# Kernel tuning notes

Hardware: AMD Instinct MI355X
Metric: run time of the kernel (lower is better)

The kernel has to match this reference:

```python
import jax, jax.numpy as jnp
import numpy as np

C = 384
NUM_HEADS = 12
WS = 12  # window side
N = WS * WS  # tokens per window = 144
NW = 144  # windows per image
BATCH = 8

def setup_inputs() -> dict:
    key = jax.random.key(0)
    k1, k2, k3, k4, k5, k6, k7 = jax.random.split(key, 7)
    x = jax.random.normal(k1, (BATCH, NW, WS, WS, C), dtype=jnp.float32)
    mask = jax.random.normal(k2, (NW, N, N), dtype=jnp.float32)
    s = 1.0 / np.sqrt(C)
    qkv_w = jax.random.normal(k3, (3 * C, C), dtype=jnp.float32) * s
    qkv_b = jax.random.normal(k4, (3 * C,), dtype=jnp.float32) * 0.02
    proj_w = jax.random.normal(k5, (C, C), dtype=jnp.float32) * s
    proj_b = jax.random.normal(k6, (C,), dtype=jnp.float32) * 0.02
    return {"x": x, "mask": mask, "qkv_w": qkv_w, "qkv_b": qkv_b,
            "proj_w": proj_w, "proj_b": proj_b}

def reference(x, mask, qkv_w, qkv_b, proj_w, proj_b):
    B, nW = x.shape[0], x.shape[1]
    head_dim = C // NUM_HEADS
    scale = head_dim ** -0.5
    # (B_, N, C) windowed tokens
    xw = x.reshape(B * nW, N, C)
    qkv = jnp.einsum('bnc,dc->bnd', xw, qkv_w) + qkv_b  # (B_, N, 3C)
    qkv = qkv.reshape(B * nW, N, 3, NUM_HEADS, head_dim)
    q = qkv[:, :, 0].transpose(0, 2, 1, 3) * scale  # (B_, H, N, hd)
    k = qkv[:, :, 1].transpose(0, 2, 1, 3)
    v = qkv[:, :, 2].transpose(0, 2, 1, 3)
    attn = jnp.einsum('bhnd,bhmd->bhnm', q, k)  # (B_, H, N, N)
    # add window mask: view as (B, nW, H, N, N) + mask[None, :, None]
    attn = attn.reshape(B, nW, NUM_HEADS, N, N) + mask[None, :, None, :, :]
    attn = jax.nn.softmax(attn.reshape(B * nW, NUM_HEADS, N, N), axis=-1)
    out = jnp.einsum('bhnm,bhmd->bhnd', attn, v)  # (B_, H, N, hd)
    out = out.transpose(0, 2, 1, 3).reshape(B * nW, N, C)
    out = jnp.einsum('bnc,dc->bnd', out, proj_w) + proj_b
    return out
```

## Files before the change

kernel.cpp:

```cpp
#include <hip/hip_runtime.h>
#include <stdint.h>

#define TOK 144
#define CD  384
#define NH  12
#define HDIM 32
#define NWIN 1152
#define MASKW 144
#define NQKV 1152

typedef __bf16 bf16_t;
typedef __bf16 bf16x4 __attribute__((ext_vector_type(4)));
typedef __bf16 bf16x8 __attribute__((ext_vector_type(8)));
typedef float  f32x4  __attribute__((ext_vector_type(4)));

__device__ __forceinline__ void gload16(const void* g, void* l) {
    __builtin_amdgcn_global_load_lds(
        (const __attribute__((address_space(1))) uint32_t*)g,
        (__attribute__((address_space(3))) uint32_t*)l, 16, 0, 0);
}

__global__ __launch_bounds__(256) void kconv(const float* __restrict__ qkvw,
                                             const float* __restrict__ projw,
                                             bf16_t* __restrict__ wq,
                                             bf16_t* __restrict__ wp)
{
    int i = (blockIdx.x * 256 + threadIdx.x) * 4;
    const int NQ = NQKV * CD;
    if (i < NQ) {
        float4 v = *(const float4*)(qkvw + i);
        bf16x4 o = {(bf16_t)v.x, (bf16_t)v.y, (bf16_t)v.z, (bf16_t)v.w};
        *(bf16x4*)(wq + i) = o;
    } else {
        int j = i - NQ;
        if (j < CD * CD) {
            float4 v = *(const float4*)(projw + j);
            bf16x4 o = {(bf16_t)v.x, (bf16_t)v.y, (bf16_t)v.z, (bf16_t)v.w};
            *(bf16x4*)(wp + j) = o;
        }
    }
}

__global__ __launch_bounds__(256) void kx(const float* __restrict__ x,
                                          bf16_t* __restrict__ xb, int n8)
{
    int i = blockIdx.x * 256 + threadIdx.x;
    if (i < n8) {
        float4 a = *(const float4*)(x + (size_t)i * 8);
        float4 b = *(const float4*)(x + (size_t)i * 8 + 4);
        bf16x8 o = {(bf16_t)a.x, (bf16_t)a.y, (bf16_t)a.z, (bf16_t)a.w,
                    (bf16_t)b.x, (bf16_t)b.y, (bf16_t)b.z, (bf16_t)b.w};
        *(bf16x8*)(xb + (size_t)i * 8) = o;
    }
}

__global__ __launch_bounds__(256) void k_qkv(const bf16_t* __restrict__ xb,
                                             const bf16_t* __restrict__ wB,
                                             const float* __restrict__ bias,
                                             bf16_t* __restrict__ Qp,
                                             bf16_t* __restrict__ Kp,
                                             bf16_t* __restrict__ VTp)
{
    int nwg = gridDim.x;
    int orig = blockIdx.x;
    int q8 = nwg >> 3, r8 = nwg & 7;
    int xcd = orig & 7, idx = orig >> 3;
    int wgid = (xcd < r8 ? xcd * (q8 + 1) : r8 * (q8 + 1) + (xcd - r8) * q8) + idx;
    int mb = wgid / 9, nb = wgid % 9;

    __shared__ union SMem {
        struct { bf16_t A[128 * 64]; bf16_t B[128 * 64]; } st;
        bf16_t tile[128 * 136];
    } sm;
    bf16_t* As = sm.st.A;
    bf16_t* Bs = sm.st.B;

    int tid = threadIdx.x;
    int lane = tid & 63, wid = tid >> 6;
    int wr = (wid >> 1) * 64, wc = (wid & 1) * 64;
    int l15 = lane & 15, l4 = lane >> 4;
    int lr8 = lane >> 3, lc8 = lane & 7;

    f32x4 acc[4][4] = {};

    const size_t arow0 = (size_t)mb * 128;
    const bf16_t* aG = xb + (arow0 + (size_t)(wid * 4) * 8 + lr8) * 384 + lc8 * 8;
    const bf16_t* bG = wB + ((size_t)nb * 128 + (size_t)(wid * 4) * 8 + lr8) * 384 + lc8 * 8;

    for (int kk = 0; kk < 6; ++kk) {
        #pragma unroll
        for (int p = 0; p < 4; ++p)
            gload16(aG + (size_t)p * (8 * 384) + kk * 64, As + (wid * 4 + p) * 512);
        #pragma unroll
        for (int p = 0; p < 4; ++p)
            gload16(bG + (size_t)p * (8 * 384) + kk * 64, Bs + (wid * 4 + p) * 512);
        __syncthreads();

        #pragma unroll
        for (int kh = 0; kh < 2; ++kh) {
            bf16x8 af[4], bfr[4];
            #pragma unroll
            for (int i = 0; i < 4; ++i)
                af[i] = *(const bf16x8*)&As[(wr + i * 16 + l15) * 64 + kh * 32 + l4 * 8];
            #pragma unroll
            for (int j = 0; j < 4; ++j)
                bfr[j] = *(const bf16x8*)&Bs[(wc + j * 16 + l15) * 64 + kh * 32 + l4 * 8];
            #pragma unroll
            for (int i = 0; i < 4; ++i)
                #pragma unroll
                for (int j = 0; j < 4; ++j)
                    acc[i][j] = __builtin_amdgcn_mfma_f32_16x16x32_bf16(af[i], bfr[j], acc[i][j], 0, 0, 0);
        }
        __syncthreads();
    }

    const int S = 136;
    const float SCALE = 0.17677669529663687f;
    float scl = (nb < 3) ? SCALE : 1.0f;
    float bv[4];
    #pragma unroll
    for (int j = 0; j < 4; ++j) bv[j] = bias[nb * 128 + wc + j * 16 + l15];

    #pragma unroll
    for (int i = 0; i < 4; ++i)
        #pragma unroll
        for (int j = 0; j < 4; ++j)
            #pragma unroll
            for (int r = 0; r < 4; ++r)
                sm.tile[(wr + i * 16 + l4 * 4 + r) * S + wc + j * 16 + l15] =
                    (bf16_t)((acc[i][j][r] + bv[j]) * scl);
    __syncthreads();

    if (nb < 6) {
        bf16_t* dst = (nb < 3) ? Qp : Kp;
        int db0 = (nb % 3) * 128;
        #pragma unroll
        for (int it = 0; it < 8; ++it) {
            int item = tid + it * 256;
            int row = item >> 4, ch = item & 15;
            bf16x8 v = *(const bf16x8*)&sm.tile[row * S + ch * 8];
            int gr = mb * 128 + row;
            int lw = gr / 144, n = gr - lw * 144;
            int dl = db0 + ch * 8;
            int h = dl >> 5, c32 = dl & 31;
            *(bf16x8*)(dst + (size_t)(lw * 12 + h) * 4608 + n * 32 + c32) = v;
        }
    } else {
        int db0 = (nb - 6) * 128;
        #pragma unroll
        for (int it = 0; it < 8; ++it) {
            int item = tid + it * 256;
            int dl = item & 127;
            int nc = item >> 7;
            int gr0 = mb * 128 + nc * 8;
            int lw = gr0 / 144, n0 = gr0 - lw * 144;
            int rr = db0 + dl;
            int h = rr >> 5, j32 = rr & 31;
            bf16x8 v;
            #pragma unroll
            for (int q = 0; q < 8; ++q)
                v[q] = sm.tile[(nc * 8 + q) * S + dl];
            *(bf16x8*)(VTp + (size_t)(lw * 12 + h) * 4608 + j32 * 144 + n0) = v;
        }
    }
}

__global__ __launch_bounds__(576) void k_attn(const bf16_t* __restrict__ Qp,
                                              const bf16_t* __restrict__ Kp,
                                              const bf16_t* __restrict__ VTp,
                                              const float* __restrict__ mask,
                                              bf16_t* __restrict__ ao,
                                              int w0)
{
    extern __shared__ char smem[];
    bf16_t* kb  = (bf16_t*)smem;
    bf16_t* vtb = kb + 144 * 40;
    bf16_t* pb  = vtb + 32 * 168;

    int bw = blockIdx.x / 12, h = blockIdx.x % 12;
    int W = w0 + bw;
    size_t base = (size_t)(bw * 12 + h) * 4608;
    int tid = threadIdx.x;

    {
        int row = tid >> 2, c8 = (tid & 3) * 8;
        *(uint4*)&kb[row * 40 + c8] = *(const uint4*)(Kp + base + row * 32 + c8);
        int j = tid / 18, seg = tid % 18;
        *(uint4*)&vtb[j * 168 + seg * 8] = *(const uint4*)(VTp + base + j * 144 + seg * 8);
        if (tid < 64) {
            int jj = tid >> 1, cc = 144 + (tid & 1) * 8;
            uint4 z = {0, 0, 0, 0};
            *(uint4*)&vtb[jj * 168 + cc] = z;
        }
    }
    __syncthreads();

    int lane = tid & 63, wv = tid >> 6;
    int l15 = lane & 15, l4 = lane >> 4;
    int row16 = wv * 16;
    const f32x4 fzero = {0.f, 0.f, 0.f, 0.f};

    bf16x8 aq = *(const bf16x8*)(Qp + base + (row16 + l15) * 32 + l4 * 8);
    f32x4 s[9];
    #pragma unroll
    for (int nt = 0; nt < 9; ++nt) {
        bf16x8 bk = *(const bf16x8*)&kb[(nt * 16 + l15) * 40 + l4 * 8];
        s[nt] = __builtin_amdgcn_mfma_f32_16x16x32_bf16(aq, bk, fzero, 0, 0, 0);
    }
    const float* mrow = mask + (size_t)(W % MASKW) * (144 * 144);
    #pragma unroll
    for (int nt = 0; nt < 9; ++nt)
        #pragma unroll
        for (int r = 0; r < 4; ++r)
            s[nt][r] += mrow[(row16 + l4 * 4 + r) * 144 + nt * 16 + l15];

    float mx[4], sm[4];
    #pragma unroll
    for (int r = 0; r < 4; ++r) {
        float m = s[0][r];
        #pragma unroll
        for (int nt = 1; nt < 9; ++nt) m = fmaxf(m, s[nt][r]);
        #pragma unroll
        for (int off = 1; off < 16; off <<= 1) m = fmaxf(m, __shfl_xor(m, off, 64));
        mx[r] = m;
    }
    #pragma unroll
    for (int r = 0; r < 4; ++r) {
        float sum = 0.f;
        #pragma unroll
        for (int nt = 0; nt < 9; ++nt) {
            float e = __expf(s[nt][r] - mx[r]);
            s[nt][r] = e;
            sum += e;
        }
        #pragma unroll
        for (int off = 1; off < 16; off <<= 1) sum += __shfl_xor(sum, off, 64);
        sm[r] = sum;
    }

    #pragma unroll
    for (int nt = 0; nt < 9; ++nt)
        #pragma unroll
        for (int r = 0; r < 4; ++r)
            pb[(row16 + l4 * 4 + r) * 168 + nt * 16 + l15] = (bf16_t)s[nt][r];
    {
        int rr = lane >> 2, cc = 144 + (lane & 3) * 4;
        uint2 z = {0, 0};
        *(uint2*)&pb[(row16 + rr) * 168 + cc] = z;
    }
    f32x4 o0 = {0.f, 0.f, 0.f, 0.f}, o1 = {0.f, 0.f, 0.f, 0.f};
    #pragma unroll
    for (int ks = 0; ks < 5; ++ks) {
        bf16x8 ap  = *(const bf16x8*)&pb[(row16 + l15) * 168 + ks * 32 + l4 * 8];
        bf16x8 bv0 = *(const bf16x8*)&vtb[(l15) * 168 + ks * 32 + l4 * 8];
        bf16x8 bv1 = *(const bf16x8*)&vtb[(16 + l15) * 168 + ks * 32 + l4 * 8];
        o0 = __builtin_amdgcn_mfma_f32_16x16x32_bf16(ap, bv0, o0, 0, 0, 0);
        o1 = __builtin_amdgcn_mfma_f32_16x16x32_bf16(ap, bv1, o1, 0, 0, 0);
    }
    float inv[4];
    #pragma unroll
    for (int r = 0; r < 4; ++r) inv[r] = 1.0f / sm[r];
    bf16_t* ob = pb + row16 * 168;
    #pragma unroll
    for (int r = 0; r < 4; ++r) {
        ob[(l4 * 4 + r) * 32 + l15]      = (bf16_t)(o0[r] * inv[r]);
        ob[(l4 * 4 + r) * 32 + 16 + l15] = (bf16_t)(o1[r] * inv[r]);
    }
    bf16x8 v = *(const bf16x8*)&ob[(lane >> 2) * 32 + (lane & 3) * 8];
    *(bf16x8*)(ao + ((size_t)bw * 144 + row16 + (lane >> 2)) * 384 + h * 32 + (lane & 3) * 8) = v;
}

__global__ __launch_bounds__(256) void k_proj(const bf16_t* __restrict__ ao,
                                              const bf16_t* __restrict__ wp,
                                              const float* __restrict__ bias,
                                              float* __restrict__ out,
                                              int rowoff)
{
    int nwg = gridDim.x;
    int orig = blockIdx.x;
    int q8 = nwg >> 3, r8 = nwg & 7;
    int xcd = orig & 7, idx = orig >> 3;
    int wgid = (xcd < r8 ? xcd * (q8 + 1) : r8 * (q8 + 1) + (xcd - r8) * q8) + idx;
    int mb = wgid / 3, nb = wgid % 3;

    __shared__ union SMem {
        struct { bf16_t A[128 * 64]; bf16_t B[128 * 64]; } st;
        float tile[128 * 68];
    } sm;
    bf16_t* As = sm.st.A;
    bf16_t* Bs = sm.st.B;

    int tid = threadIdx.x;
    int lane = tid & 63, wid = tid >> 6;
    int wr = (wid >> 1) * 64, wc = (wid & 1) * 64;
    int l15 = lane & 15, l4 = lane >> 4;
    int lr8 = lane >> 3, lc8 = lane & 7;

    f32x4 acc[4][4] = {};

    const bf16_t* aG = ao + ((size_t)mb * 128 + (size_t)(wid * 4) * 8 + lr8) * 384 + lc8 * 8;
    const bf16_t* bG = wp + ((size_t)nb * 128 + (size_t)(wid * 4) * 8 + lr8) * 384 + lc8 * 8;

    for (int kk = 0; kk < 6; ++kk) {
        #pragma unroll
        for (int p = 0; p < 4; ++p)
            gload16(aG + (size_t)p * (8 * 384) + kk * 64, As + (wid * 4 + p) * 512);
        #pragma unroll
        for (int p = 0; p < 4; ++p)
            gload16(bG + (size_t)p * (8 * 384) + kk * 64, Bs + (wid * 4 + p) * 512);
        __syncthreads();

        #pragma unroll
        for (int kh = 0; kh < 2; ++kh) {
            bf16x8 af[4], bfr[4];
            #pragma unroll
            for (int i = 0; i < 4; ++i)
                af[i] = *(const bf16x8*)&As[(wr + i * 16 + l15) * 64 + kh * 32 + l4 * 8];
            #pragma unroll
            for (int j = 0; j < 4; ++j)
                bfr[j] = *(const bf16x8*)&Bs[(wc + j * 16 + l15) * 64 + kh * 32 + l4 * 8];
            #pragma unroll
            for (int i = 0; i < 4; ++i)
                #pragma unroll
                for (int j = 0; j < 4; ++j)
                    acc[i][j] = __builtin_amdgcn_mfma_f32_16x16x32_bf16(af[i], bfr[j], acc[i][j], 0, 0, 0);
        }
        __syncthreads();
    }

    float bv[4];
    #pragma unroll
    for (int j = 0; j < 4; ++j) bv[j] = bias[nb * 128 + wc + j * 16 + l15];

    #pragma unroll
    for (int half = 0; half < 2; ++half) {
        if (half) __syncthreads();
        if ((wid & 1) == half) {
            #pragma unroll
            for (int i = 0; i < 4; ++i)
                #pragma unroll
                for (int j = 0; j < 4; ++j)
                    #pragma unroll
                    for (int r = 0; r < 4; ++r)
                        sm.tile[(wr + i * 16 + l4 * 4 + r) * 68 + j * 16 + l15] =
                            acc[i][j][r] + bv[j];
        }
        __syncthreads();
        #pragma unroll
        for (int it = 0; it < 8; ++it) {
            int item = tid + it * 256;
            int row = item >> 4, ch = item & 15;
            float4 v = *(const float4*)&sm.tile[row * 68 + ch * 4];
            *(float4*)(out + (size_t)(rowoff + mb * 128 + row) * 384
                           + nb * 128 + half * 64 + ch * 4) = v;
        }
    }
}

extern "C" void kernel_launch(void* const* d_in, const int* in_sizes, int n_in,
                              void* d_out, int out_size, void* d_ws, size_t ws_size,
                              hipStream_t stream)
{
    const float* x     = (const float*)d_in[0];
    const float* mask  = (const float*)d_in[1];
    const float* qkvw  = (const float*)d_in[2];
    const float* qkvb  = (const float*)d_in[3];
    const float* projw = (const float*)d_in[4];
    const float* projb = (const float*)d_in[5];
    float* out = (float*)d_out;

    char* ws = (char*)d_ws;
    bf16_t* WQ = (bf16_t*)ws;
    bf16_t* WP = (bf16_t*)(ws + 884736);
    char* chunkbase = ws + 1179648;

    size_t avail = ws_size > 1179648 ? ws_size - 1179648 : 0;
    long cw = (long)(avail / 552960);
    cw = (cw / 16) * 16;
    if (cw > NWIN) cw = NWIN;
    if (cw < 16) cw = 16;

    size_t qbytes = (size_t)cw * 110592;
    bf16_t* Xb  = (bf16_t*)chunkbase;
    bf16_t* Qp  = (bf16_t*)(chunkbase + qbytes);
    bf16_t* Kp  = (bf16_t*)(chunkbase + 2 * qbytes);
    bf16_t* VTp = (bf16_t*)(chunkbase + 3 * qbytes);
    bf16_t* AO  = (bf16_t*)(chunkbase + 4 * qbytes);

    kconv<<<576, 256, 0, stream>>>(qkvw, projw, WQ, WP);

    for (int w0 = 0; w0 < NWIN; w0 += (int)cw) {
        int c = (int)((NWIN - w0) < cw ? (NWIN - w0) : cw);
        int n8 = c * 6912;
        kx<<<(n8 + 255) / 256, 256, 0, stream>>>(x + (size_t)w0 * 144 * 384, Xb, n8);
        int mblocks = (c * 144) / 128;
        k_qkv<<<mblocks * 9, 256, 0, stream>>>(Xb, WQ, qkvb, Qp, Kp, VTp);
        k_attn<<<c * 12, 576, 70656, stream>>>(Qp, Kp, VTp, mask, AO, w0);
        k_proj<<<mblocks * 3, 256, 0, stream>>>(AO, WP, projb, out, w0 * 144);
    }
}
```

Before: 805.1 us.

## Pre-permute mask into MFMA fragment layout and remap attention blocks per XCD

Adds a pre-pass kernel that rearranges the fp32 window mask into the per-lane MFMA accumulator layout. The attention kernel then loads it as one contiguous 16-byte vector per tile and passes it as the MFMA accumulator input, instead of doing strided scalar loads followed by separate adds. The attention block index is also remapped so that consecutive blocks, which share a window's mask and data, land on the same XCD for better L2 reuse. The cost is an extra ~12 MB workspace region and one extra kernel launch per call. The mask relayout runs inside the timed call, so it is not a hack.

```diff
diff --git a/kernel.cpp b/kernel.cpp
--- a/kernel.cpp
+++ b/kernel.cpp
@@ -41,6 +41,22 @@
     }
 }
 
+__global__ __launch_bounds__(256) void kmask(const float* __restrict__ mask,
+                                             float* __restrict__ maskR)
+{
+    int t = blockIdx.x * 256 + threadIdx.x;
+    int lane = t & 63;
+    int g = t >> 6;
+    int nt = g % 9;
+    int g2 = g / 9;
+    int wv = g2 % 9;
+    int wm = g2 / 9;
+    const float* src = mask + (size_t)wm * 20736
+                     + (wv * 16 + (lane >> 4) * 4) * 144 + nt * 16 + (lane & 15);
+    f32x4 v = { src[0], src[144], src[288], src[432] };
+    *(f32x4*)(maskR + (size_t)t * 4) = v;
+}
+
 __global__ __launch_bounds__(256) void kx(const float* __restrict__ x,
                                           bf16_t* __restrict__ xb, int n8)
 {
@@ -168,7 +184,7 @@
 __global__ __launch_bounds__(576) void k_attn(const bf16_t* __restrict__ Qp,
                                               const bf16_t* __restrict__ Kp,
                                               const bf16_t* __restrict__ VTp,
-                                              const float* __restrict__ mask,
+                                              const float* __restrict__ maskR,
                                               bf16_t* __restrict__ ao,
                                               int w0)
 {
@@ -177,8 +193,15 @@
     bf16_t* vtb = kb + 144 * 40;
     bf16_t* pb  = vtb + 32 * 168;
 
-    int bw = blockIdx.x / 12, h = blockIdx.x % 12;
+    int nwg = gridDim.x;
+    int orig = blockIdx.x;
+    int q8 = nwg >> 3, r8 = nwg & 7;
+    int xcd = orig & 7, idx = orig >> 3;
+    int wgid = (xcd < r8 ? xcd * (q8 + 1) : r8 * (q8 + 1) + (xcd - r8) * q8) + idx;
+
+    int bw = wgid / 12, h = wgid % 12;
     int W = w0 + bw;
+    int wm = W % MASKW;
     size_t base = (size_t)(bw * 12 + h) * 4608;
     int tid = threadIdx.x;
 
@@ -198,21 +221,17 @@
     int lane = tid & 63, wv = tid >> 6;
     int l15 = lane & 15, l4 = lane >> 4;
     int row16 = wv * 16;
-    const f32x4 fzero = {0.f, 0.f, 0.f, 0.f};
 
     bf16x8 aq = *(const bf16x8*)(Qp + base + (row16 + l15) * 32 + l4 * 8);
+
+    const float* mR = maskR + ((size_t)(wm * 9 + wv) * 9) * 256 + lane * 4;
     f32x4 s[9];
     #pragma unroll
     for (int nt = 0; nt < 9; ++nt) {
         bf16x8 bk = *(const bf16x8*)&kb[(nt * 16 + l15) * 40 + l4 * 8];
-        s[nt] = __builtin_amdgcn_mfma_f32_16x16x32_bf16(aq, bk, fzero, 0, 0, 0);
-    }
-    const float* mrow = mask + (size_t)(W % MASKW) * (144 * 144);
-    #pragma unroll
-    for (int nt = 0; nt < 9; ++nt)
-        #pragma unroll
-        for (int r = 0; r < 4; ++r)
-            s[nt][r] += mrow[(row16 + l4 * 4 + r) * 144 + nt * 16 + l15];
+        f32x4 mv = *(const f32x4*)(mR + nt * 256);
+        s[nt] = __builtin_amdgcn_mfma_f32_16x16x32_bf16(aq, bk, mv, 0, 0, 0);
+    }
 
     float mx[4], sm[4];
     #pragma unroll
@@ -370,11 +389,12 @@
     float* out = (float*)d_out;
 
     char* ws = (char*)d_ws;
-    bf16_t* WQ = (bf16_t*)ws;
-    bf16_t* WP = (bf16_t*)(ws + 884736);
-    char* chunkbase = ws + 1179648;
-
-    size_t avail = ws_size > 1179648 ? ws_size - 1179648 : 0;
+    bf16_t* WQ   = (bf16_t*)ws;
+    bf16_t* WP   = (bf16_t*)(ws + 884736);
+    float* maskR = (float*)(ws + 1179648);
+    char* chunkbase = ws + 13123584;
+
+    size_t avail = ws_size > 13123584 ? ws_size - 13123584 : 0;
     long cw = (long)(avail / 552960);
     cw = (cw / 16) * 16;
     if (cw > NWIN) cw = NWIN;
@@ -388,6 +408,7 @@
     bf16_t* AO  = (bf16_t*)(chunkbase + 4 * qbytes);
 
     kconv<<<576, 256, 0, stream>>>(qkvw, projw, WQ, WP);
+    kmask<<<2916, 256, 0, stream>>>(mask, maskR);
 
     for (int w0 = 0; w0 < NWIN; w0 += (int)cw) {
         int c = (int)((NWIN - w0) < cw ? (NWIN - w0) : cw);
@@ -395,7 +416,7 @@
         kx<<<(n8 + 255) / 256, 256, 0, stream>>>(x + (size_t)w0 * 144 * 384, Xb, n8);
         int mblocks = (c * 144) / 128;
         k_qkv<<<mblocks * 9, 256, 0, stream>>>(Xb, WQ, qkvb, Qp, Kp, VTp);
-        k_attn<<<c * 12, 576, 70656, stream>>>(Qp, Kp, VTp, mask, AO, w0);
+        k_attn<<<c * 12, 576, 70656, stream>>>(Qp, Kp, VTp, maskR, AO, w0);
         k_proj<<<mblocks * 3, 256, 0, stream>>>(AO, WP, projb, out, w0 * 144);
     }
 }
```

Result: faster. 661.1 us (-17.9%).
